# Performance work log

Hardware: AMD Instinct MI355X
Metric: run time of the kernel (lower is better)

## Reference

```python
import jax, jax.numpy as jnp
import numpy as np
from jax import lax

T, N, F, H, E = 8, 20000, 128, 256, 320000
LEAK = 0.9


def setup_inputs() -> dict:
    key = jax.random.key(0)
    k = jax.random.split(key, 7)
    x = jax.random.normal(k[0], (T, N, F), dtype=jnp.float32)
    edge_index = jax.random.randint(k[1], (2, E), 0, N, dtype=jnp.int32)
    # reservoir weights, scaled ~1/sqrt(fan_in) so tanh stays in its active range
    w_in0 = jax.random.normal(k[2], (H, F), dtype=jnp.float32) / jnp.sqrt(F)
    w_rec0 = jax.random.normal(k[3], (H, H), dtype=jnp.float32) / jnp.sqrt(H)
    w_in1 = jax.random.normal(k[4], (H, H), dtype=jnp.float32) / jnp.sqrt(H)
    w_rec1 = jax.random.normal(k[5], (H, H), dtype=jnp.float32) / jnp.sqrt(H)
    leakage = jnp.array(LEAK, dtype=jnp.float32)
    return {"x": x, "edge_index": edge_index, "w_in0": w_in0, "w_rec0": w_rec0,
            "w_in1": w_in1, "w_rec1": w_rec1, "leakage": leakage}


def reference(x, edge_index, w_in0, w_rec0, w_in1, w_rec1, leakage):
    # DynamicGraphReservoir with 2 ReservoirConvLayers, fixed graph over time,
    # zero initial states, no pooling, fully=False, return_sequences=False.
    src, dst = edge_index[0], edge_index[1]
    num_nodes = x.shape[1]

    def layer(w_in, w_rec, inp, state):
        # neighbour aggregation: sum_{(j->i) in E} state[j]   (scatter-add)
        agg = jax.ops.segment_sum(state[src], dst, num_segments=num_nodes)
        return leakage * jnp.tanh(inp @ w_in.T + agg @ w_rec.T) + (1.0 - leakage) * state

    def step(states, xt):
        s0, s1 = states
        s0 = layer(w_in0, w_rec0, xt, s0)   # layer 0 consumes input signal
        s1 = layer(w_in1, w_rec1, s0, s1)   # layer 1 consumes layer-0 state
        return (s0, s1), None

    init = (jnp.zeros((num_nodes, w_rec0.shape[0]), x.dtype),
            jnp.zeros((num_nodes, w_rec1.shape[0]), x.dtype))
    (s0, s1), _ = lax.scan(step, init, x)
    return s1  # final-layer final state: (nodes, hidden)
```

## Files before the change

kernel.cpp:

```cpp
#include <hip/hip_runtime.h>
#include <math.h>

#define T_STEPS 8
#define N_NODES 20000
#define F_IN    128
#define H_DIM   256
#define E_EDGES 320000

#define G_UPD    625
#define G_AGG    5000

typedef __attribute__((ext_vector_type(8))) short short8;
typedef __attribute__((ext_vector_type(4))) float f32x4;

__device__ __forceinline__ void split2(float v, unsigned short& h, unsigned short& l) {
    unsigned vi = __float_as_uint(v);
    h = (unsigned short)(vi >> 16);
    float hf = __uint_as_float(vi & 0xffff0000u);
    l = (unsigned short)(__float_as_uint(v - hf) >> 16);
}


__global__ void count_kernel(const int* __restrict__ dst, int* __restrict__ counts, int E) {
    int e = blockIdx.x * blockDim.x + threadIdx.x;
    if (e < E) atomicAdd(&counts[dst[e]], 1);
}

__global__ void scan_kernel(const int* __restrict__ counts, int* __restrict__ row_ptr,
                            int* __restrict__ cursors, int n) {
    __shared__ int buf[1024];
    __shared__ int carry_s;
    int tid = threadIdx.x;
    if (tid == 0) carry_s = 0;
    __syncthreads();
    for (int base = 0; base < n; base += 1024) {
        int i = base + tid;
        int v = (i < n) ? counts[i] : 0;
        buf[tid] = v;
        __syncthreads();
        for (int off = 1; off < 1024; off <<= 1) {
            int t = (tid >= off) ? buf[tid - off] : 0;
            __syncthreads();
            buf[tid] += t;
            __syncthreads();
        }
        int incl = buf[tid];
        int carry = carry_s;
        if (i < n) {
            int ex = carry + incl - v;
            row_ptr[i] = ex;
            cursors[i] = ex;
        }
        __syncthreads();
        if (tid == 1023) carry_s = carry + incl;
        __syncthreads();
    }
    if (tid == 0) row_ptr[n] = carry_s;
}

__global__ void fill_kernel(const int* __restrict__ src, const int* __restrict__ dst,
                            int* __restrict__ cursors, unsigned short* __restrict__ col, int E) {
    int e = blockIdx.x * blockDim.x + threadIdx.x;
    if (e < E) {
        int d = dst[e];
        int p = atomicAdd(&cursors[d], 1);
        col[p] = (unsigned short)src[e];
    }
}


__global__ void cvt_frag(const float* __restrict__ W, int K,
                         unsigned short* __restrict__ fh, unsigned short* __restrict__ fl) {
    int g = blockIdx.x * 256 + threadIdx.x;
    int KP32 = K >> 5;
    int total = (H_DIM / 16) * KP32 * 64;
    if (g >= total) return;
    int lane = g & 63;
    int kp = (g >> 6) % KP32;
    int rt = g / (KP32 << 6);
    int r = rt * 16 + (lane & 15);
    int c = kp * 32 + (lane >> 4) * 8;
    const float* p = W + (size_t)r * K + c;
    short8 h, l;
    #pragma unroll
    for (int j = 0; j < 8; ++j) {
        unsigned short hh, ll;
        split2(p[j], hh, ll);
        h[j] = (short)hh; l[j] = (short)ll;
    }
    *(short8*)(fh + (size_t)g * 8) = h;
    *(short8*)(fl + (size_t)g * 8) = l;
}


__global__ __launch_bounds__(256) void agg_kernel(
        const float* __restrict__ gsrc, float* __restrict__ gout,
        const int* __restrict__ row_ptr, const unsigned short* __restrict__ col) {
    const int tid = threadIdx.x;
    const int lane = tid & 63, w = tid >> 6;
    const int g = blockIdx.x;
    const int chunk = g & 7;
    const int nb = g >> 3;
    const int slot = lane >> 3, comp = lane & 7;
    const float4* src4 = (const float4*)gsrc + (size_t)chunk * 8 + comp;
    #pragma unroll 1
    for (int i = 0; i < 8; ++i) {
        int r = nb * 32 + w * 8 + i;
        int beg = row_ptr[r], end = row_ptr[r + 1];
        float4 a = {0.f, 0.f, 0.f, 0.f};
        int j = beg + slot;
        for (; j + 8 < end; j += 16) {
            int i0 = col[j];
            int i1 = col[j + 8];
            float4 v0 = src4[(size_t)i0 * 64];
            float4 v1 = src4[(size_t)i1 * 64];
            a.x += v0.x; a.y += v0.y; a.z += v0.z; a.w += v0.w;
            a.x += v1.x; a.y += v1.y; a.z += v1.z; a.w += v1.w;
        }
        if (j < end) {
            int i0 = col[j];
            float4 v0 = src4[(size_t)i0 * 64];
            a.x += v0.x; a.y += v0.y; a.z += v0.z; a.w += v0.w;
        }
        #pragma unroll
        for (int m = 8; m < 64; m <<= 1) {
            a.x += __shfl_xor(a.x, m);
            a.y += __shfl_xor(a.y, m);
            a.z += __shfl_xor(a.z, m);
            a.w += __shfl_xor(a.w, m);
        }
        if (slot == 0)
            *(float4*)(gout + (size_t)r * 256 + chunk * 32 + comp * 4) = a;
    }
}


__device__ __forceinline__ void upd_body(
        const float* __restrict__ A1, int K1,
        const float* __restrict__ s_prev,
        const unsigned short* __restrict__ B1h, const unsigned short* __restrict__ B1l,
        const unsigned short* __restrict__ B2h, const unsigned short* __restrict__ B2l,
        const float* __restrict__ AGGu,
        float* __restrict__ s_new,
        const float* __restrict__ leak_ptr, int m0) {
    const int tid = threadIdx.x;
    const int lane = tid & 63, w = tid >> 6;
    const int fr = lane & 15, fq = lane >> 4;
    const int wn = w * 64;
    const int rtbase = w * 4;

    f32x4 acc[2][4];
    #pragma unroll
    for (int mi = 0; mi < 2; ++mi)
        #pragma unroll
        for (int nt = 0; nt < 4; ++nt)
            acc[mi][nt] = (f32x4){0.f, 0.f, 0.f, 0.f};

    {
        const int KP32 = K1 >> 5;
        #pragma unroll 1
        for (int kp = 0; kp < KP32; ++kp) {
            short8 ah[2], al[2];
            #pragma unroll
            for (int mi = 0; mi < 2; ++mi) {
                const float* ap = A1 + (size_t)(m0 + mi * 16 + fr) * K1 + kp * 32 + fq * 8;
                float4 v0 = *(const float4*)ap;
                float4 v1 = *(const float4*)(ap + 4);
                unsigned short h, l;
                split2(v0.x, h, l); ah[mi][0] = (short)h; al[mi][0] = (short)l;
                split2(v0.y, h, l); ah[mi][1] = (short)h; al[mi][1] = (short)l;
                split2(v0.z, h, l); ah[mi][2] = (short)h; al[mi][2] = (short)l;
                split2(v0.w, h, l); ah[mi][3] = (short)h; al[mi][3] = (short)l;
                split2(v1.x, h, l); ah[mi][4] = (short)h; al[mi][4] = (short)l;
                split2(v1.y, h, l); ah[mi][5] = (short)h; al[mi][5] = (short)l;
                split2(v1.z, h, l); ah[mi][6] = (short)h; al[mi][6] = (short)l;
                split2(v1.w, h, l); ah[mi][7] = (short)h; al[mi][7] = (short)l;
            }
            short8 bh[4], bl[4];
            #pragma unroll
            for (int nt = 0; nt < 4; ++nt) {
                size_t off = ((size_t)((rtbase + nt) * KP32 + kp) * 64 + lane) * 8;
                bh[nt] = *(const short8*)(B1h + off);
                bl[nt] = *(const short8*)(B1l + off);
            }
            #pragma unroll
            for (int mi = 0; mi < 2; ++mi)
                #pragma unroll
                for (int nt = 0; nt < 4; ++nt) {
                    f32x4 c = acc[mi][nt];
                    c = __builtin_amdgcn_mfma_f32_16x16x32_bf16(ah[mi], bh[nt], c, 0, 0, 0);
                    c = __builtin_amdgcn_mfma_f32_16x16x32_bf16(al[mi], bh[nt], c, 0, 0, 0);
                    c = __builtin_amdgcn_mfma_f32_16x16x32_bf16(ah[mi], bl[nt], c, 0, 0, 0);
                    acc[mi][nt] = c;
                }
        }
    }

    if (B2h) {
        #pragma unroll 1
        for (int kp = 0; kp < 8; ++kp) {
            short8 ah[2], al[2];
            #pragma unroll
            for (int mi = 0; mi < 2; ++mi) {
                const float* ap = AGGu + (size_t)(m0 + mi * 16 + fr) * H_DIM + kp * 32 + fq * 8;
                float4 v0 = *(const float4*)ap;
                float4 v1 = *(const float4*)(ap + 4);
                unsigned short h, l;
                split2(v0.x, h, l); ah[mi][0] = (short)h; al[mi][0] = (short)l;
                split2(v0.y, h, l); ah[mi][1] = (short)h; al[mi][1] = (short)l;
                split2(v0.z, h, l); ah[mi][2] = (short)h; al[mi][2] = (short)l;
                split2(v0.w, h, l); ah[mi][3] = (short)h; al[mi][3] = (short)l;
                split2(v1.x, h, l); ah[mi][4] = (short)h; al[mi][4] = (short)l;
                split2(v1.y, h, l); ah[mi][5] = (short)h; al[mi][5] = (short)l;
                split2(v1.z, h, l); ah[mi][6] = (short)h; al[mi][6] = (short)l;
                split2(v1.w, h, l); ah[mi][7] = (short)h; al[mi][7] = (short)l;
            }
            short8 bh[4], bl[4];
            #pragma unroll
            for (int nt = 0; nt < 4; ++nt) {
                size_t off = ((size_t)((rtbase + nt) * 8 + kp) * 64 + lane) * 8;
                bh[nt] = *(const short8*)(B2h + off);
                bl[nt] = *(const short8*)(B2l + off);
            }
            #pragma unroll
            for (int mi = 0; mi < 2; ++mi)
                #pragma unroll
                for (int nt = 0; nt < 4; ++nt) {
                    f32x4 c = acc[mi][nt];
                    c = __builtin_amdgcn_mfma_f32_16x16x32_bf16(ah[mi], bh[nt], c, 0, 0, 0);
                    c = __builtin_amdgcn_mfma_f32_16x16x32_bf16(al[mi], bh[nt], c, 0, 0, 0);
                    c = __builtin_amdgcn_mfma_f32_16x16x32_bf16(ah[mi], bl[nt], c, 0, 0, 0);
                    acc[mi][nt] = c;
                }
        }
    }

    const float leak = leak_ptr[0], il = 1.0f - leak;
    #pragma unroll
    for (int mi = 0; mi < 2; ++mi)
        #pragma unroll
        for (int r = 0; r < 4; ++r) {
            int m = m0 + mi * 16 + fq * 4 + r;
            #pragma unroll
            for (int nt = 0; nt < 4; ++nt) {
                int n = wn + nt * 16 + fr;
                size_t idx = (size_t)m * H_DIM + n;
                float old = s_prev[idx];
                float pre = acc[mi][nt][r];
                float e = __expf(2.0f * pre);
                float th = 1.0f - 2.0f / (e + 1.0f);
                s_new[idx] = leak * th + il * old;
            }
        }
}

__global__ __launch_bounds__(256) void upd_kernel(
        const float* __restrict__ A1a, int K1a, const float* __restrict__ spa,
        const unsigned short* __restrict__ B1ha, const unsigned short* __restrict__ B1la,
        const unsigned short* __restrict__ B2ha, const unsigned short* __restrict__ B2la,
        const float* __restrict__ AGGa, float* __restrict__ sna,
        const float* __restrict__ A1b, int K1b, const float* __restrict__ spb,
        const unsigned short* __restrict__ B1hb, const unsigned short* __restrict__ B1lb,
        const unsigned short* __restrict__ B2hb, const unsigned short* __restrict__ B2lb,
        const float* __restrict__ AGGb, float* __restrict__ snb,
        const float* __restrict__ leak_ptr, int merged) {
    if (merged) {
        const int task = blockIdx.x & 1;
        const int m0 = (blockIdx.x >> 1) * 32;
        if (task == 0)
            upd_body(A1a, K1a, spa, B1ha, B1la, B2ha, B2la, AGGa, sna, leak_ptr, m0);
        else
            upd_body(A1b, K1b, spb, B1hb, B1lb, B2hb, B2lb, AGGb, snb, leak_ptr, m0);
    } else {
        upd_body(A1a, K1a, spa, B1ha, B1la, B2ha, B2la, AGGa, sna, leak_ptr, blockIdx.x * 32);
    }
}


extern "C" void kernel_launch(void* const* d_in, const int* in_sizes, int n_in,
                              void* d_out, int out_size, void* d_ws, size_t ws_size,
                              hipStream_t stream) {
    const float* x        = (const float*)d_in[0];
    const int*   edge     = (const int*)d_in[1];
    const float* w_in0    = (const float*)d_in[2];
    const float* w_rec0   = (const float*)d_in[3];
    const float* w_in1    = (const float*)d_in[4];
    const float* w_rec1   = (const float*)d_in[5];
    const float* leak_ptr = (const float*)d_in[6];

    const int* src = edge;
    const int* dst = edge + E_EDGES;

    char* ws = (char*)d_ws;
    size_t off = 0;
    auto alloc = [&](size_t bytes) -> char* {
        char* p = ws + off;
        off += (bytes + 255) & ~(size_t)255;
        return p;
    };
    const size_t state_bytes = (size_t)N_NODES * H_DIM * sizeof(float);
    float* s0b[2]; float* s1b[2];
    s0b[0] = (float*)alloc(state_bytes);
    s0b[1] = (float*)alloc(state_bytes);
    s1b[0] = (float*)d_out;
    s1b[1] = (float*)alloc(state_bytes);
    float* AGG0 = (float*)alloc(state_bytes);
    float* AGG1 = (float*)alloc(state_bytes);
    unsigned short* w0h  = (unsigned short*)alloc(256 * 128 * 2);
    unsigned short* w0l  = (unsigned short*)alloc(256 * 128 * 2);
    unsigned short* wr0h = (unsigned short*)alloc(256 * 256 * 2);
    unsigned short* wr0l = (unsigned short*)alloc(256 * 256 * 2);
    unsigned short* w1h  = (unsigned short*)alloc(256 * 256 * 2);
    unsigned short* w1l  = (unsigned short*)alloc(256 * 256 * 2);
    unsigned short* wr1h = (unsigned short*)alloc(256 * 256 * 2);
    unsigned short* wr1l = (unsigned short*)alloc(256 * 256 * 2);
    int* row_ptr = (int*)alloc((N_NODES + 1) * sizeof(int));
    int* cursors = (int*)alloc(N_NODES * sizeof(int));
    int* counts  = (int*)alloc(N_NODES * sizeof(int));
    unsigned short* col = (unsigned short*)alloc((size_t)E_EDGES * sizeof(unsigned short));

    hipMemsetAsync(s0b[0], 0, state_bytes, stream);
    hipMemsetAsync(s1b[0], 0, state_bytes, stream);
    hipMemsetAsync(counts, 0, N_NODES * sizeof(int), stream);

    cvt_frag<<<16, 256, 0, stream>>>(w_in0, F_IN, w0h, w0l);
    cvt_frag<<<32, 256, 0, stream>>>(w_rec0, H_DIM, wr0h, wr0l);
    cvt_frag<<<32, 256, 0, stream>>>(w_in1, H_DIM, w1h, w1l);
    cvt_frag<<<32, 256, 0, stream>>>(w_rec1, H_DIM, wr1h, wr1l);

    count_kernel<<<(E_EDGES + 255) / 256, 256, 0, stream>>>(dst, counts, E_EDGES);
    scan_kernel<<<1, 1024, 0, stream>>>(counts, row_ptr, cursors, N_NODES);
    fill_kernel<<<(E_EDGES + 255) / 256, 256, 0, stream>>>(src, dst, cursors, col, E_EDGES);

    dim3 g_upd1(G_UPD);
    dim3 g_upd2(2 * G_UPD);
    dim3 g_agg(G_AGG);


    upd_kernel<<<g_upd1, 256, 0, stream>>>(
        x, F_IN, s0b[0], w0h, w0l, nullptr, nullptr, nullptr, s0b[1],
        nullptr, 0, nullptr, nullptr, nullptr, nullptr, nullptr, nullptr, nullptr,
        leak_ptr, 0);
    agg_kernel<<<g_agg, 256, 0, stream>>>(s0b[1], AGG0, row_ptr, col);

    for (int t = 0; t < 7; ++t) {
        const float* s0_t  = s0b[(t + 1) & 1];
        float* s0_n        = s0b[t & 1];
        const float* s1_p  = s1b[t & 1];
        float* s1_t        = s1b[(t + 1) & 1];
        const float* xt1 = x + (size_t)(t + 1) * N_NODES * F_IN;
        int dg1 = (t > 0) ? 1 : 0;

        upd_kernel<<<g_upd2, 256, 0, stream>>>(
            s0_t, H_DIM, s1_p, w1h, w1l,
            dg1 ? wr1h : nullptr, dg1 ? wr1l : nullptr, AGG1, s1_t,
            xt1, F_IN, s0_t, w0h, w0l, wr0h, wr0l, AGG0, s0_n,
            leak_ptr, 1);

        agg_kernel<<<g_agg, 256, 0, stream>>>(s1_t, AGG1, row_ptr, col);
        if (t + 2 <= 7)
            agg_kernel<<<g_agg, 256, 0, stream>>>(s0_n, AGG0, row_ptr, col);
    }

    upd_kernel<<<g_upd1, 256, 0, stream>>>(
        s0b[0], H_DIM, s1b[1], w1h, w1l, wr1h, wr1l, AGG1, s1b[0],
        nullptr, 0, nullptr, nullptr, nullptr, nullptr, nullptr, nullptr, nullptr,
        leak_ptr, 0);
}
```

Before: 1.251 ms.

## Batch agg gathers across rows, merge paired agg launches, prefetch GEMM A tiles

The aggregation kernel now walks all 8 rows of a wave together, issuing 8 independent column and gather loads per iteration to raise memory-level parallelism, instead of processing rows one after another. The two aggregation launches per timestep are merged into one grid of twice the size, with each block selecting its source and output buffer from its block index. The update GEMM loops register-prefetch the next k-slice of the fp32 A operand before converting the current one to split bf16. This adds register pressure and predicated wasted loads when row lengths are uneven.

```diff
diff --git a/kernel.cpp b/kernel.cpp
--- a/kernel.cpp
+++ b/kernel.cpp
@@ -94,43 +94,66 @@
 
 
 __global__ __launch_bounds__(256) void agg_kernel(
-        const float* __restrict__ gsrc, float* __restrict__ gout,
+        const float* __restrict__ gsrcA, float* __restrict__ goutA,
+        const float* __restrict__ gsrcB, float* __restrict__ goutB,
         const int* __restrict__ row_ptr, const unsigned short* __restrict__ col) {
+    int b = blockIdx.x;
+    const float* gsrc = gsrcA;
+    float* gout = goutA;
+    if (b >= G_AGG) { b -= G_AGG; gsrc = gsrcB; gout = goutB; }
     const int tid = threadIdx.x;
     const int lane = tid & 63, w = tid >> 6;
-    const int g = blockIdx.x;
-    const int chunk = g & 7;
-    const int nb = g >> 3;
+    const int chunk = b & 7;
+    const int nb = b >> 3;
     const int slot = lane >> 3, comp = lane & 7;
     const float4* src4 = (const float4*)gsrc + (size_t)chunk * 8 + comp;
-    #pragma unroll 1
-    for (int i = 0; i < 8; ++i) {
-        int r = nb * 32 + w * 8 + i;
-        int beg = row_ptr[r], end = row_ptr[r + 1];
-        float4 a = {0.f, 0.f, 0.f, 0.f};
-        int j = beg + slot;
-        for (; j + 8 < end; j += 16) {
-            int i0 = col[j];
-            int i1 = col[j + 8];
-            float4 v0 = src4[(size_t)i0 * 64];
-            float4 v1 = src4[(size_t)i1 * 64];
-            a.x += v0.x; a.y += v0.y; a.z += v0.z; a.w += v0.w;
-            a.x += v1.x; a.y += v1.y; a.z += v1.z; a.w += v1.w;
-        }
-        if (j < end) {
-            int i0 = col[j];
-            float4 v0 = src4[(size_t)i0 * 64];
-            a.x += v0.x; a.y += v0.y; a.z += v0.z; a.w += v0.w;
-        }
+    const int r0 = nb * 32 + w * 8;
+
+    int jj[8], en[8];
+    float4 ac[8];
+    #pragma unroll
+    for (int k = 0; k < 8; ++k) {
+        jj[k] = row_ptr[r0 + k] + slot;
+        en[k] = row_ptr[r0 + k + 1];
+        ac[k] = (float4){0.f, 0.f, 0.f, 0.f};
+    }
+    while (true) {
+        bool ok[8];
+        int ix[8];
+        bool anyv = false;
+        #pragma unroll
+        for (int k = 0; k < 8; ++k) {
+            ok[k] = jj[k] < en[k];
+            anyv |= ok[k];
+            ix[k] = ok[k] ? jj[k] : 0;
+        }
+        if (!anyv) break;
+        int cc[8];
+        #pragma unroll
+        for (int k = 0; k < 8; ++k) cc[k] = col[ix[k]];
+        #pragma unroll
+        for (int k = 0; k < 8; ++k) {
+            float4 v = src4[(size_t)cc[k] * 64];
+            if (ok[k]) {
+                ac[k].x += v.x; ac[k].y += v.y; ac[k].z += v.z; ac[k].w += v.w;
+                jj[k] += 8;
+            }
+        }
+    }
+    #pragma unroll
+    for (int k = 0; k < 8; ++k) {
         #pragma unroll
         for (int m = 8; m < 64; m <<= 1) {
-            a.x += __shfl_xor(a.x, m);
-            a.y += __shfl_xor(a.y, m);
-            a.z += __shfl_xor(a.z, m);
-            a.w += __shfl_xor(a.w, m);
-        }
-        if (slot == 0)
-            *(float4*)(gout + (size_t)r * 256 + chunk * 32 + comp * 4) = a;
+            ac[k].x += __shfl_xor(ac[k].x, m);
+            ac[k].y += __shfl_xor(ac[k].y, m);
+            ac[k].z += __shfl_xor(ac[k].z, m);
+            ac[k].w += __shfl_xor(ac[k].w, m);
+        }
+    }
+    if (slot == 0) {
+        #pragma unroll
+        for (int k = 0; k < 8; ++k)
+            *(float4*)(gout + (size_t)(r0 + k) * 256 + chunk * 32 + comp * 4) = ac[k];
     }
 }
 
@@ -158,30 +181,46 @@
 
     {
         const int KP32 = K1 >> 5;
+        const float* ar0 = A1 + (size_t)(m0 + fr) * K1 + fq * 8;
+        const float* ar1 = A1 + (size_t)(m0 + 16 + fr) * K1 + fq * 8;
+        float4 pA0, pA1, pB0, pB1;
+        pA0 = *(const float4*)ar0;
+        pA1 = *(const float4*)(ar0 + 4);
+        pB0 = *(const float4*)ar1;
+        pB1 = *(const float4*)(ar1 + 4);
         #pragma unroll 1
         for (int kp = 0; kp < KP32; ++kp) {
-            short8 ah[2], al[2];
-            #pragma unroll
-            for (int mi = 0; mi < 2; ++mi) {
-                const float* ap = A1 + (size_t)(m0 + mi * 16 + fr) * K1 + kp * 32 + fq * 8;
-                float4 v0 = *(const float4*)ap;
-                float4 v1 = *(const float4*)(ap + 4);
-                unsigned short h, l;
-                split2(v0.x, h, l); ah[mi][0] = (short)h; al[mi][0] = (short)l;
-                split2(v0.y, h, l); ah[mi][1] = (short)h; al[mi][1] = (short)l;
-                split2(v0.z, h, l); ah[mi][2] = (short)h; al[mi][2] = (short)l;
-                split2(v0.w, h, l); ah[mi][3] = (short)h; al[mi][3] = (short)l;
-                split2(v1.x, h, l); ah[mi][4] = (short)h; al[mi][4] = (short)l;
-                split2(v1.y, h, l); ah[mi][5] = (short)h; al[mi][5] = (short)l;
-                split2(v1.z, h, l); ah[mi][6] = (short)h; al[mi][6] = (short)l;
-                split2(v1.w, h, l); ah[mi][7] = (short)h; al[mi][7] = (short)l;
-            }
+            const int kpn = (kp + 1 < KP32) ? kp + 1 : kp;
+            float4 nA0 = *(const float4*)(ar0 + kpn * 32);
+            float4 nA1 = *(const float4*)(ar0 + kpn * 32 + 4);
+            float4 nB0 = *(const float4*)(ar1 + kpn * 32);
+            float4 nB1 = *(const float4*)(ar1 + kpn * 32 + 4);
             short8 bh[4], bl[4];
             #pragma unroll
             for (int nt = 0; nt < 4; ++nt) {
                 size_t off = ((size_t)((rtbase + nt) * KP32 + kp) * 64 + lane) * 8;
                 bh[nt] = *(const short8*)(B1h + off);
                 bl[nt] = *(const short8*)(B1l + off);
+            }
+            short8 ah[2], al[2];
+            {
+                unsigned short h, l;
+                split2(pA0.x, h, l); ah[0][0] = (short)h; al[0][0] = (short)l;
+                split2(pA0.y, h, l); ah[0][1] = (short)h; al[0][1] = (short)l;
+                split2(pA0.z, h, l); ah[0][2] = (short)h; al[0][2] = (short)l;
+                split2(pA0.w, h, l); ah[0][3] = (short)h; al[0][3] = (short)l;
+                split2(pA1.x, h, l); ah[0][4] = (short)h; al[0][4] = (short)l;
+                split2(pA1.y, h, l); ah[0][5] = (short)h; al[0][5] = (short)l;
+                split2(pA1.z, h, l); ah[0][6] = (short)h; al[0][6] = (short)l;
+                split2(pA1.w, h, l); ah[0][7] = (short)h; al[0][7] = (short)l;
+                split2(pB0.x, h, l); ah[1][0] = (short)h; al[1][0] = (short)l;
+                split2(pB0.y, h, l); ah[1][1] = (short)h; al[1][1] = (short)l;
+                split2(pB0.z, h, l); ah[1][2] = (short)h; al[1][2] = (short)l;
+                split2(pB0.w, h, l); ah[1][3] = (short)h; al[1][3] = (short)l;
+                split2(pB1.x, h, l); ah[1][4] = (short)h; al[1][4] = (short)l;
+                split2(pB1.y, h, l); ah[1][5] = (short)h; al[1][5] = (short)l;
+                split2(pB1.z, h, l); ah[1][6] = (short)h; al[1][6] = (short)l;
+                split2(pB1.w, h, l); ah[1][7] = (short)h; al[1][7] = (short)l;
             }
             #pragma unroll
             for (int mi = 0; mi < 2; ++mi)
@@ -193,34 +232,51 @@
                     c = __builtin_amdgcn_mfma_f32_16x16x32_bf16(ah[mi], bl[nt], c, 0, 0, 0);
                     acc[mi][nt] = c;
                 }
+            pA0 = nA0; pA1 = nA1; pB0 = nB0; pB1 = nB1;
         }
     }
 
     if (B2h) {
+        const float* ar0 = AGGu + (size_t)(m0 + fr) * H_DIM + fq * 8;
+        const float* ar1 = AGGu + (size_t)(m0 + 16 + fr) * H_DIM + fq * 8;
+        float4 pA0, pA1, pB0, pB1;
+        pA0 = *(const float4*)ar0;
+        pA1 = *(const float4*)(ar0 + 4);
+        pB0 = *(const float4*)ar1;
+        pB1 = *(const float4*)(ar1 + 4);
         #pragma unroll 1
         for (int kp = 0; kp < 8; ++kp) {
-            short8 ah[2], al[2];
-            #pragma unroll
-            for (int mi = 0; mi < 2; ++mi) {
-                const float* ap = AGGu + (size_t)(m0 + mi * 16 + fr) * H_DIM + kp * 32 + fq * 8;
-                float4 v0 = *(const float4*)ap;
-                float4 v1 = *(const float4*)(ap + 4);
-                unsigned short h, l;
-                split2(v0.x, h, l); ah[mi][0] = (short)h; al[mi][0] = (short)l;
-                split2(v0.y, h, l); ah[mi][1] = (short)h; al[mi][1] = (short)l;
-                split2(v0.z, h, l); ah[mi][2] = (short)h; al[mi][2] = (short)l;
-                split2(v0.w, h, l); ah[mi][3] = (short)h; al[mi][3] = (short)l;
-                split2(v1.x, h, l); ah[mi][4] = (short)h; al[mi][4] = (short)l;
-                split2(v1.y, h, l); ah[mi][5] = (short)h; al[mi][5] = (short)l;
-                split2(v1.z, h, l); ah[mi][6] = (short)h; al[mi][6] = (short)l;
-                split2(v1.w, h, l); ah[mi][7] = (short)h; al[mi][7] = (short)l;
-            }
+            const int kpn = (kp + 1 < 8) ? kp + 1 : kp;
+            float4 nA0 = *(const float4*)(ar0 + kpn * 32);
+            float4 nA1 = *(const float4*)(ar0 + kpn * 32 + 4);
+            float4 nB0 = *(const float4*)(ar1 + kpn * 32);
+            float4 nB1 = *(const float4*)(ar1 + kpn * 32 + 4);
             short8 bh[4], bl[4];
             #pragma unroll
             for (int nt = 0; nt < 4; ++nt) {
                 size_t off = ((size_t)((rtbase + nt) * 8 + kp) * 64 + lane) * 8;
                 bh[nt] = *(const short8*)(B2h + off);
                 bl[nt] = *(const short8*)(B2l + off);
+            }
+            short8 ah[2], al[2];
+            {
+                unsigned short h, l;
+                split2(pA0.x, h, l); ah[0][0] = (short)h; al[0][0] = (short)l;
+                split2(pA0.y, h, l); ah[0][1] = (short)h; al[0][1] = (short)l;
+                split2(pA0.z, h, l); ah[0][2] = (short)h; al[0][2] = (short)l;
+                split2(pA0.w, h, l); ah[0][3] = (short)h; al[0][3] = (short)l;
+                split2(pA1.x, h, l); ah[0][4] = (short)h; al[0][4] = (short)l;
+                split2(pA1.y, h, l); ah[0][5] = (short)h; al[0][5] = (short)l;
+                split2(pA1.z, h, l); ah[0][6] = (short)h; al[0][6] = (short)l;
+                split2(pA1.w, h, l); ah[0][7] = (short)h; al[0][7] = (short)l;
+                split2(pB0.x, h, l); ah[1][0] = (short)h; al[1][0] = (short)l;
+                split2(pB0.y, h, l); ah[1][1] = (short)h; al[1][1] = (short)l;
+                split2(pB0.z, h, l); ah[1][2] = (short)h; al[1][2] = (short)l;
+                split2(pB0.w, h, l); ah[1][3] = (short)h; al[1][3] = (short)l;
+                split2(pB1.x, h, l); ah[1][4] = (short)h; al[1][4] = (short)l;
+                split2(pB1.y, h, l); ah[1][5] = (short)h; al[1][5] = (short)l;
+                split2(pB1.z, h, l); ah[1][6] = (short)h; al[1][6] = (short)l;
+                split2(pB1.w, h, l); ah[1][7] = (short)h; al[1][7] = (short)l;
             }
             #pragma unroll
             for (int mi = 0; mi < 2; ++mi)
@@ -232,6 +288,7 @@
                     c = __builtin_amdgcn_mfma_f32_16x16x32_bf16(ah[mi], bl[nt], c, 0, 0, 0);
                     acc[mi][nt] = c;
                 }
+            pA0 = nA0; pA1 = nA1; pB0 = nB0; pB1 = nB1;
         }
     }
 
@@ -334,14 +391,15 @@
 
     dim3 g_upd1(G_UPD);
     dim3 g_upd2(2 * G_UPD);
-    dim3 g_agg(G_AGG);
+    dim3 g_agg1(G_AGG);
+    dim3 g_agg2(2 * G_AGG);
 
 
     upd_kernel<<<g_upd1, 256, 0, stream>>>(
         x, F_IN, s0b[0], w0h, w0l, nullptr, nullptr, nullptr, s0b[1],
         nullptr, 0, nullptr, nullptr, nullptr, nullptr, nullptr, nullptr, nullptr,
         leak_ptr, 0);
-    agg_kernel<<<g_agg, 256, 0, stream>>>(s0b[1], AGG0, row_ptr, col);
+    agg_kernel<<<g_agg1, 256, 0, stream>>>(s0b[1], AGG0, nullptr, nullptr, row_ptr, col);
 
     for (int t = 0; t < 7; ++t) {
         const float* s0_t  = s0b[(t + 1) & 1];
@@ -357,9 +415,11 @@
             xt1, F_IN, s0_t, w0h, w0l, wr0h, wr0l, AGG0, s0_n,
             leak_ptr, 1);
 
-        agg_kernel<<<g_agg, 256, 0, stream>>>(s1_t, AGG1, row_ptr, col);
-        if (t + 2 <= 7)
-            agg_kernel<<<g_agg, 256, 0, stream>>>(s0_n, AGG0, row_ptr, col);
+        if (t < 6) {
+            agg_kernel<<<g_agg2, 256, 0, stream>>>(s1_t, AGG1, s0_n, AGG0, row_ptr, col);
+        } else {
+            agg_kernel<<<g_agg1, 256, 0, stream>>>(s1_t, AGG1, nullptr, nullptr, row_ptr, col);
+        }
     }
 
     upd_kernel<<<g_upd1, 256, 0, stream>>>(
```

Measured after the change: 1.298 ms. 3.8% more time.
